# Kernel tuning notes

Measured on AMD Instinct MI355X. Metric: run time of the kernel, lower is better.

Reference implementation:

```python
import jax, jax.numpy as jnp
import numpy as np

B, LS, VS = 4, 1024, 1024
VH, LH, H = 1024, 1024, 16
HD = LH // H  # head_dim = 64


def setup_inputs() -> dict:
    key = jax.random.key(0)
    ks = jax.random.split(key, 10)
    s = 0.02
    return {
        "v_hidden_states": jax.random.normal(ks[0], (B, VS, VH), jnp.float32),
        "l_hidden_states": jax.random.normal(ks[1], (B, LS, LH), jnp.float32),
        "q_w": jax.random.normal(ks[2], (LH, LH), jnp.float32) * s,
        "q_b": jnp.zeros((LH,), jnp.float32),
        "k_w": jax.random.normal(ks[3], (VH, LH), jnp.float32) * s,
        "k_b": jnp.zeros((LH,), jnp.float32),
        "v_w": jax.random.normal(ks[4], (VH, LH), jnp.float32) * s,
        "v_b": jnp.zeros((LH,), jnp.float32),
        "o_w": jax.random.normal(ks[5], (LH, LH), jnp.float32) * s,
        "o_b": jnp.zeros((LH,), jnp.float32),
    }


def reference(v_hidden_states, l_hidden_states, q_w, q_b, k_w, k_b, v_w, v_b, o_w, o_b):
    b, ls, _ = l_hidden_states.shape
    vs = v_hidden_states.shape[1]
    q = (l_hidden_states @ q_w + q_b).reshape(b, ls, H, HD)
    k = (v_hidden_states @ k_w + k_b).reshape(b, vs, H, HD)
    v = (v_hidden_states @ v_w + v_b).reshape(b, vs, H, HD)
    # NOTE: original scales by sqrt(hidden_size), not sqrt(head_dim)
    scale = jnp.sqrt(jnp.asarray(LH, q.dtype))
    scores = jnp.einsum("blhd,bvhd->bhlv", q, k) / scale
    attn = jax.nn.softmax(scores, axis=-1)
    out = jnp.einsum("bhlv,bvhd->blhd", attn, v).reshape(b, ls, LH)
    return out @ o_w + o_b
```

## Files before the change

kernel.cpp:

```cpp
#include <hip/hip_runtime.h>

typedef __bf16 bf16;
typedef __attribute__((ext_vector_type(4))) __bf16 bf16x4;
typedef __attribute__((ext_vector_type(8))) __bf16 bf16x8;
typedef __attribute__((ext_vector_type(4))) float f32x4;

static __device__ __forceinline__ f32x4 mfma_16x16x32(bf16x8 a, bf16x8 b, f32x4 c) {
    return __builtin_amdgcn_mfma_f32_16x16x32_bf16(a, b, c, 0, 0, 0);
}

static __device__ __forceinline__ bf16x8 load8(const float* p) {
    f32x4 a = *(const f32x4*)p;
    f32x4 b = *(const f32x4*)(p + 4);
    bf16x8 r;
    r[0] = (bf16)a[0]; r[1] = (bf16)a[1]; r[2] = (bf16)a[2]; r[3] = (bf16)a[3];
    r[4] = (bf16)b[0]; r[5] = (bf16)b[1]; r[6] = (bf16)b[2]; r[7] = (bf16)b[3];
    return r;
}

static __device__ __forceinline__ void gload_lds16(const void* g, void* l) {
    __builtin_amdgcn_global_load_lds(
        (const __attribute__((address_space(1))) void*)g,
        (__attribute__((address_space(3))) void*)l, 16, 0, 0);
}

#define QSCALE 0.0450842200277801f

#define SYNC_PRE(N)                                                      \
    do {                                                                 \
        asm volatile("s_waitcnt vmcnt(" #N ")" ::: "memory");            \
        __builtin_amdgcn_s_barrier();                                    \
        __builtin_amdgcn_sched_barrier(0);                               \
    } while (0)

#define SYNC_POST()                                                     \
    do {                                                                \
        asm volatile("s_waitcnt lgkmcnt(0)" ::: "memory");              \
        __builtin_amdgcn_sched_barrier(0);                              \
        __builtin_amdgcn_s_barrier();                                   \
    } while (0)

__global__ __launch_bounds__(256) void prep_kernel(
    const float* __restrict__ l_h, const float* __restrict__ v_h,
    const float* __restrict__ w0, const float* __restrict__ w1,
    const float* __restrict__ w2, const float* __restrict__ w3,
    bf16* __restrict__ l_bf, bf16* __restrict__ v_bf,
    bf16* __restrict__ dq, bf16* __restrict__ dkv, bf16* __restrict__ dov)
{
    const int id = blockIdx.x;
    if (id < 4096) {
        const float* s = (id < 2048) ? l_h : v_h;
        bf16*       d = (id < 2048) ? l_bf : v_bf;
        const int   bb = (id < 2048) ? id : id - 2048;
        const size_t i = ((size_t)bb * 256 + threadIdx.x) * 8;
        *(bf16x8*)(d + i) = load8(s + i);
        return;
    }
    const int widx = id - 4096;
    const int z    = widx >> 8;
    const int rem  = widx & 255;
    const int j0   = (rem & 15) * 64;
    const int i0   = (rem >> 4) * 64;
    const float* src; bf16* dst;
    switch (z) {
        case 0:  src = w0; dst = dq; break;
        case 1:  src = w1; dst = dkv; break;
        case 2:  src = w2; dst = dkv + (size_t)1024 * 1024; break;
        default: src = w3; dst = dov; break;
    }
    const float wscale = (z == 0) ? QSCALE : 1.0f;
    __shared__ float T[64][65];
    const int tx = threadIdx.x & 15;
    const int ty = threadIdx.x >> 4;
    #pragma unroll
    for (int it = 0; it < 4; ++it) {
        f32x4 v = *(const f32x4*)(src + (size_t)(i0 + ty + it * 16) * 1024 + j0 + tx * 4);
        T[ty + it * 16][tx * 4 + 0] = v[0];
        T[ty + it * 16][tx * 4 + 1] = v[1];
        T[ty + it * 16][tx * 4 + 2] = v[2];
        T[ty + it * 16][tx * 4 + 3] = v[3];
    }
    __syncthreads();
    #pragma unroll
    for (int it = 0; it < 4; ++it) {
        const int jj = ty + it * 16;
        bf16x4 o;
        o[0] = (bf16)(T[tx * 4 + 0][jj] * wscale);
        o[1] = (bf16)(T[tx * 4 + 1][jj] * wscale);
        o[2] = (bf16)(T[tx * 4 + 2][jj] * wscale);
        o[3] = (bf16)(T[tx * 4 + 3][jj] * wscale);
        *(bf16x4*)(dst + (size_t)(j0 + jj) * 1024 + i0 + tx * 4) = o;
    }
}

__global__ __launch_bounds__(512, 2) void proj256_kernel(
    const bf16* __restrict__ l_bf, const bf16* __restrict__ v_bf,
    const bf16* __restrict__ QWt,  const bf16* __restrict__ KVWt,
    const float* __restrict__ q_b, const float* __restrict__ k_b,
    const float* __restrict__ v_b,
    bf16* __restrict__ Qh, bf16* __restrict__ Kh, bf16* __restrict__ Vt)
{
    __shared__ __align__(16) bf16 Asl[2][256][64];
    __shared__ __align__(16) bf16 Bsl[2][256][64];

    const int t    = threadIdx.x;
    const int lane = t & 63;
    const int wave = t >> 6;
    const int wm   = wave & 1;
    const int wn   = wave >> 1;
    const int l15  = lane & 15;
    const int quad = lane >> 4;
    const int swz  = l15 & 7;

    const int orig = blockIdx.x;
    const int wg   = (orig & 7) * 24 + (orig >> 3);
    const int by   = wg / 12;
    const int bx   = wg - by * 12;

    const bool isQ = bx < 4;
    const bf16* Ap = isQ ? l_bf : v_bf;
    const bf16* Bt = isQ ? QWt  : KVWt;
    const int  gn0 = (isQ ? bx : bx - 4) * 256;
    const int  gm0 = by * 256;

    const int srow8 = t >> 3;
    const int gch   = (t & 7) ^ (srow8 & 7);
    const size_t abase = (size_t)(gm0 + srow8) * 1024 + gch * 8;
    const size_t bbase = (size_t)(gn0 + srow8) * 1024 + gch * 8;

    f32x4 acc[8][4];
    #pragma unroll
    for (int i = 0; i < 8; ++i)
        #pragma unroll
        for (int j = 0; j < 4; ++j)
            acc[i][j] = (f32x4){0.f, 0.f, 0.f, 0.f};

    #define STG(kt_, b_)                                                           \
        {                                                                          \
            _Pragma("unroll")                                                      \
            for (int q = 0; q < 4; ++q)                                            \
                gload_lds16(Ap + abase + (size_t)q * 64 * 1024 + (kt_) * 64,       \
                            &Asl[b_][q * 64 + wave * 8][0]);                       \
            _Pragma("unroll")                                                      \
            for (int q = 0; q < 4; ++q)                                            \
                gload_lds16(Bt + bbase + (size_t)q * 64 * 1024 + (kt_) * 64,       \
                            &Bsl[b_][q * 64 + wave * 8][0]);                       \
        }

    #define CTILE(b_)                                                              \
        {                                                                          \
            bf16x8 bfv[4][2], af[4][2];                                            \
            _Pragma("unroll")                                                      \
            for (int nt = 0; nt < 4; ++nt)                                         \
                _Pragma("unroll")                                                  \
                for (int kk = 0; kk < 2; ++kk)                                     \
                    bfv[nt][kk] = *(const bf16x8*)(&Bsl[b_][wn * 64 + nt * 16 + l15] \
                                                        [((kk * 4 + quad) ^ swz) * 8]); \
            _Pragma("unroll")                                                      \
            for (int i = 0; i < 4; ++i)                                            \
                _Pragma("unroll")                                                  \
                for (int kk = 0; kk < 2; ++kk)                                     \
                    af[i][kk] = *(const bf16x8*)(&Asl[b_][wm * 128 + i * 16 + l15] \
                                                      [((kk * 4 + quad) ^ swz) * 8]); \
            __builtin_amdgcn_s_setprio(1);                                         \
            _Pragma("unroll")                                                      \
            for (int i = 0; i < 4; ++i)                                            \
                _Pragma("unroll")                                                  \
                for (int nt = 0; nt < 4; ++nt)                                     \
                    _Pragma("unroll")                                              \
                    for (int kk = 0; kk < 2; ++kk)                                 \
                        acc[i][nt] = mfma_16x16x32(af[i][kk], bfv[nt][kk], acc[i][nt]); \
            __builtin_amdgcn_s_setprio(0);                                         \
            _Pragma("unroll")                                                      \
            for (int i = 0; i < 4; ++i)                                            \
                _Pragma("unroll")                                                  \
                for (int kk = 0; kk < 2; ++kk)                                     \
                    af[i][kk] = *(const bf16x8*)(&Asl[b_][wm * 128 + 64 + i * 16 + l15] \
                                                      [((kk * 4 + quad) ^ swz) * 8]); \
            __builtin_amdgcn_s_setprio(1);                                         \
            _Pragma("unroll")                                                      \
            for (int i = 0; i < 4; ++i)                                            \
                _Pragma("unroll")                                                  \
                for (int nt = 0; nt < 4; ++nt)                                     \
                    _Pragma("unroll")                                              \
                    for (int kk = 0; kk < 2; ++kk)                                 \
                        acc[4 + i][nt] = mfma_16x16x32(af[i][kk], bfv[nt][kk], acc[4 + i][nt]); \
            __builtin_amdgcn_s_setprio(0);                                         \
        }

    STG(0, 0);
    STG(1, 1);
    asm volatile("s_waitcnt vmcnt(8)" ::: "memory");
    __builtin_amdgcn_s_barrier();

    for (int tt = 0; tt < 14; ++tt) {
        const int b = tt & 1;
        CTILE(b);
        __builtin_amdgcn_s_barrier();
        STG(tt + 2, b);
        asm volatile("s_waitcnt vmcnt(8)" ::: "memory");
        __builtin_amdgcn_s_barrier();
    }
    CTILE(0);
    __builtin_amdgcn_s_barrier();
    asm volatile("s_waitcnt vmcnt(0)" ::: "memory");
    __builtin_amdgcn_s_barrier();
    CTILE(1);

    #undef STG
    #undef CTILE

    #pragma unroll
    for (int nt = 0; nt < 4; ++nt) {
        const int col = gn0 + wn * 64 + nt * 16 + l15;
        float bb; bf16* dst; bool hm;
        if (isQ)             { bb = q_b[col] * QSCALE;   dst = Qh; hm = true;  }
        else if (col < 1024) { bb = k_b[col];            dst = Kh; hm = true;  }
        else                 { bb = v_b[col - 1024];     dst = Vt; hm = false; }
        #pragma unroll
        for (int mt = 0; mt < 8; ++mt) {
            #pragma unroll
            for (int r = 0; r < 4; ++r) {
                const int row = gm0 + wm * 128 + mt * 16 + quad * 4 + r;
                const float v = acc[mt][nt][r] + bb;
                if (hm) {
                    const size_t idx =
                        ((size_t)((row >> 10) * 16 + (col >> 6)) * 1024 +
                         (row & 1023)) * 64 + (col & 63);
                    dst[idx] = (bf16)v;
                } else {
                    const int vc = col - 1024;
                    const size_t idx =
                        ((size_t)((row >> 10) * 16 + (vc >> 6)) * 64 +
                         (vc & 63)) * 1024 + (row & 1023);
                    dst[idx] = (bf16)v;
                }
            }
        }
    }
}

__global__ __launch_bounds__(256, 3) void ogemm_kernel(
    const bf16* __restrict__ Aw, const bf16* __restrict__ OWt,
    const float* __restrict__ o_b, float* __restrict__ C)
{
    __shared__ __align__(16) bf16 As[3][128][32];
    __shared__ __align__(16) bf16 Bs[3][64][32];

    const int t    = threadIdx.x;
    const int lane = t & 63;
    const int wave = t >> 6;
    const int wm   = wave & 1;
    const int wn   = wave >> 1;
    const int l15  = lane & 15;
    const int quad = lane >> 4;

    const int orig = blockIdx.y * 16 + blockIdx.x;
    const int wg   = (orig & 7) * 64 + (orig >> 3);
    const int by   = wg >> 4;
    const int bx   = wg & 15;

    const int gn0 = bx * 64;
    const int gm0 = by * 128;
    const int K   = 1024;

    const int srow    = lane >> 2;
    const int chunk_g = (lane & 3) ^ ((srow >> 1) & 3);
    const size_t aoff = (size_t)(gm0 + wave * 32 + srow) * K + chunk_g * 8;
    const size_t boff = (size_t)(gn0 + wave * 16 + srow) * K + chunk_g * 8;

    f32x4 acc[4][2];
    #pragma unroll
    for (int i = 0; i < 4; ++i)
        #pragma unroll
        for (int j = 0; j < 2; ++j)
            acc[i][j] = (f32x4){0.f, 0.f, 0.f, 0.f};

    #define OSTAGE(k0_, buf_)                                                          \
        {                                                                              \
            gload_lds16(Aw + aoff + (k0_),                  &As[buf_][wave * 32][0]);  \
            gload_lds16(Aw + aoff + (size_t)16 * K + (k0_), &As[buf_][wave * 32 + 16][0]); \
            gload_lds16(OWt + boff + (k0_),                 &Bs[buf_][wave * 16][0]);  \
        }

    #define OCOMPUTE(bufi)                                                             \
        {                                                                              \
            bf16x8 af[4], bfr[2];                                                      \
            _Pragma("unroll")                                                          \
            for (int mt = 0; mt < 4; ++mt) {                                           \
                const int row = wm * 64 + mt * 16 + l15;                               \
                af[mt] = *(const bf16x8*)(&As[bufi][row][(quad ^ ((row >> 1) & 3)) * 8]); \
            }                                                                          \
            _Pragma("unroll")                                                          \
            for (int nt = 0; nt < 2; ++nt) {                                           \
                const int row = wn * 32 + nt * 16 + l15;                               \
                bfr[nt] = *(const bf16x8*)(&Bs[bufi][row][(quad ^ ((row >> 1) & 3)) * 8]); \
            }                                                                          \
            __builtin_amdgcn_s_setprio(1);                                             \
            _Pragma("unroll")                                                          \
            for (int mt = 0; mt < 4; ++mt)                                             \
                _Pragma("unroll")                                                      \
                for (int nt = 0; nt < 2; ++nt)                                         \
                    acc[mt][nt] = mfma_16x16x32(af[mt], bfr[nt], acc[mt][nt]);         \
            __builtin_amdgcn_s_setprio(0);                                             \
        }

    OSTAGE(0, 0);
    OSTAGE(32, 1);
    int bc = 0, bn2 = 2;

    for (int k0 = 0; k0 < K - 64; k0 += 32) {
        OSTAGE(k0 + 64, bn2);
        SYNC_PRE(6);
        OCOMPUTE(bc);
        SYNC_POST();
        int nb = bc + 1;  if (nb == 3) nb = 0;
        int nn = bn2 + 1; if (nn == 3) nn = 0;
        bc = nb; bn2 = nn;
    }
    SYNC_PRE(3);
    OCOMPUTE(bc);
    SYNC_POST();
    bc = (bc + 1 == 3) ? 0 : bc + 1;
    SYNC_PRE(0);
    OCOMPUTE(bc);

    #undef OSTAGE
    #undef OCOMPUTE

    #pragma unroll
    for (int nt = 0; nt < 2; ++nt) {
        const int col = gn0 + wn * 32 + nt * 16 + l15;
        const float bb = o_b[col];
        #pragma unroll
        for (int mt = 0; mt < 4; ++mt) {
            #pragma unroll
            for (int r = 0; r < 4; ++r) {
                const int row = gm0 + wm * 64 + mt * 16 + quad * 4 + r;
                C[(size_t)row * 1024 + col] = acc[mt][nt][r] + bb;
            }
        }
    }
}

__global__ __launch_bounds__(256) void attn_kernel(
    const bf16* __restrict__ Q, const bf16* __restrict__ K,
    const bf16* __restrict__ V, bf16* __restrict__ O)
{
    const int t    = threadIdx.x;
    const int lane = t & 63;
    const int wave = t >> 6;
    const int l15  = lane & 15;
    const int quad = lane >> 4;

    const int head = blockIdx.x;
    const int q0   = blockIdx.y * 128;
    const int b    = head >> 4;
    const int h    = head & 15;

    __shared__ __align__(16) bf16 Kb[2][64][64];
    __shared__ __align__(16) bf16 Vb[2][64][64];
    __shared__ __align__(16) bf16 P[4][32][72];

    const bf16* Qp  = Q + ((size_t)head * 1024 + q0 + wave * 32) * 64;
    const bf16* Kp  = K + (size_t)head * 1024 * 64;
    const bf16* Vtp = V + (size_t)head * 64 * 1024;

    const int r8  = lane >> 3;
    const int c8  = lane & 7;
    const int swz = (c8 ^ r8) * 8;

    bf16x8 aq[2][2];
    #pragma unroll
    for (int mt = 0; mt < 2; ++mt)
        #pragma unroll
        for (int kc = 0; kc < 2; ++kc)
            aq[mt][kc] = *(const bf16x8*)(Qp + (mt * 16 + l15) * 64 + kc * 32 + quad * 8);

    bf16x8 vones;
    #pragma unroll
    for (int j = 0; j < 8; ++j) vones[j] = (bf16)1.0f;

    f32x4 oacc[2][4];
    #pragma unroll
    for (int mt = 0; mt < 2; ++mt)
        #pragma unroll
        for (int nt = 0; nt < 4; ++nt)
            oacc[mt][nt] = (f32x4){0.f, 0.f, 0.f, 0.f};
    f32x4 lacc[2];
    lacc[0] = (f32x4){0.f, 0.f, 0.f, 0.f};
    lacc[1] = (f32x4){0.f, 0.f, 0.f, 0.f};

    #define STAGE(c, buf)                                                          \
        {                                                                          \
            const int kv0_ = (c) * 64;                                             \
            _Pragma("unroll")                                                      \
            for (int g = 0; g < 2; ++g) {                                          \
                const int R = wave * 16 + g * 8;                                   \
                gload_lds16(Kp + (size_t)(kv0_ + R + r8) * 64 + swz,               \
                            &Kb[buf][R][0]);                                       \
                gload_lds16(Vtp + (size_t)(R + r8) * 1024 + kv0_ + swz,            \
                            &Vb[buf][R][0]);                                       \
            }                                                                      \
        }

    STAGE(0, 0);

    const int sw = l15 & 7;

    for (int c = 0; c < 16; ++c) {
        const int buf = c & 1;
        __syncthreads();
        if (c + 1 < 16) STAGE(c + 1, buf ^ 1);

        #pragma unroll
        for (int nt = 0; nt < 4; ++nt) {
            const bf16* krow = &Kb[buf][nt * 16 + l15][0];
            bf16x8 bk0 = *(const bf16x8*)(krow + (quad ^ sw) * 8);
            bf16x8 bk1 = *(const bf16x8*)(krow + ((quad + 4) ^ sw) * 8);
            #pragma unroll
            for (int mt = 0; mt < 2; ++mt) {
                f32x4 s = (f32x4){0.f, 0.f, 0.f, 0.f};
                s = mfma_16x16x32(aq[mt][0], bk0, s);
                s = mfma_16x16x32(aq[mt][1], bk1, s);
                #pragma unroll
                for (int r = 0; r < 4; ++r) {
                    const float e = __builtin_amdgcn_exp2f(s[r]);
                    P[wave][mt * 16 + quad * 4 + r][nt * 16 + l15] = (bf16)e;
                }
            }
        }

        #pragma unroll
        for (int mt = 0; mt < 2; ++mt) {
            bf16x8 pa0 = *(const bf16x8*)(&P[wave][mt * 16 + l15][quad * 8]);
            bf16x8 pa1 = *(const bf16x8*)(&P[wave][mt * 16 + l15][32 + quad * 8]);
            lacc[mt] = mfma_16x16x32(pa0, vones, lacc[mt]);
            lacc[mt] = mfma_16x16x32(pa1, vones, lacc[mt]);
            #pragma unroll
            for (int nt = 0; nt < 4; ++nt) {
                const bf16* vrow = &Vb[buf][nt * 16 + l15][0];
                bf16x8 bv0 = *(const bf16x8*)(vrow + (quad ^ sw) * 8);
                bf16x8 bv1 = *(const bf16x8*)(vrow + ((quad + 4) ^ sw) * 8);
                oacc[mt][nt] = mfma_16x16x32(pa0, bv0, oacc[mt][nt]);
                oacc[mt][nt] = mfma_16x16x32(pa1, bv1, oacc[mt][nt]);
            }
        }
    }
    #undef STAGE

    #pragma unroll
    for (int mt = 0; mt < 2; ++mt) {
        const float invs[4] = {1.0f / lacc[mt][0], 1.0f / lacc[mt][1],
                               1.0f / lacc[mt][2], 1.0f / lacc[mt][3]};
        #pragma unroll
        for (int nt = 0; nt < 4; ++nt) {
            #pragma unroll
            for (int r = 0; r < 4; ++r) {
                const int row = q0 + wave * 32 + mt * 16 + quad * 4 + r;
                O[((size_t)b * 1024 + row) * 1024 + h * 64 + nt * 16 + l15] =
                    (bf16)(oacc[mt][nt][r] * invs[r]);
            }
        }
    }
}

extern "C" void kernel_launch(void* const* d_in, const int* in_sizes, int n_in,
                              void* d_out, int out_size, void* d_ws, size_t ws_size,
                              hipStream_t stream)
{
    const float* v_h = (const float*)d_in[0];
    const float* l_h = (const float*)d_in[1];
    const float* q_w = (const float*)d_in[2];
    const float* q_b = (const float*)d_in[3];
    const float* k_w = (const float*)d_in[4];
    const float* k_b = (const float*)d_in[5];
    const float* v_w = (const float*)d_in[6];
    const float* v_b = (const float*)d_in[7];
    const float* o_w = (const float*)d_in[8];
    const float* o_b = (const float*)d_in[9];
    float* out = (float*)d_out;

    const size_t SZ = (size_t)4096 * 1024;
    const size_t WZ = (size_t)1024 * 1024;

    bf16* l_bf = (bf16*)d_ws;
    bf16* v_bf = l_bf + SZ;
    bf16* QWt  = v_bf + SZ;
    bf16* KVWt = QWt + WZ;
    bf16* OWt  = KVWt + 2 * WZ;
    bf16* Qh   = OWt + WZ;
    bf16* Kh   = Qh + SZ;
    bf16* Vt   = Kh + SZ;
    bf16* Aw   = Vt + SZ;

    prep_kernel<<<dim3(5120), 256, 0, stream>>>(
        l_h, v_h, q_w, k_w, v_w, o_w, l_bf, v_bf, QWt, KVWt, OWt);

    proj256_kernel<<<dim3(192), 512, 0, stream>>>(
        l_bf, v_bf, QWt, KVWt, q_b, k_b, v_b, Qh, Kh, Vt);

    attn_kernel<<<dim3(64, 8), 256, 0, stream>>>(Qh, Kh, Vt, Aw);

    ogemm_kernel<<<dim3(16, 32), 256, 0, stream>>>(Aw, OWt, o_b, out);

    (void)in_sizes; (void)n_in; (void)out_size; (void)ws_size;
}
```

Baseline: 212.0 us.

## Restructure QKV projection GEMM into 8-phase ping-pong schedule with interleaved loads

```diff
diff --git a/kernel.cpp b/kernel.cpp
--- a/kernel.cpp
+++ b/kernel.cpp
@@ -135,80 +135,96 @@
         for (int j = 0; j < 4; ++j)
             acc[i][j] = (f32x4){0.f, 0.f, 0.f, 0.f};
 
-    #define STG(kt_, b_)                                                           \
-        {                                                                          \
-            _Pragma("unroll")                                                      \
-            for (int q = 0; q < 4; ++q)                                            \
-                gload_lds16(Ap + abase + (size_t)q * 64 * 1024 + (kt_) * 64,       \
-                            &Asl[b_][q * 64 + wave * 8][0]);                       \
-            _Pragma("unroll")                                                      \
-            for (int q = 0; q < 4; ++q)                                            \
-                gload_lds16(Bt + bbase + (size_t)q * 64 * 1024 + (kt_) * 64,       \
-                            &Bsl[b_][q * 64 + wave * 8][0]);                       \
-        }
-
-    #define CTILE(b_)                                                              \
-        {                                                                          \
-            bf16x8 bfv[4][2], af[4][2];                                            \
-            _Pragma("unroll")                                                      \
-            for (int nt = 0; nt < 4; ++nt)                                         \
-                _Pragma("unroll")                                                  \
-                for (int kk = 0; kk < 2; ++kk)                                     \
-                    bfv[nt][kk] = *(const bf16x8*)(&Bsl[b_][wn * 64 + nt * 16 + l15] \
-                                                        [((kk * 4 + quad) ^ swz) * 8]); \
-            _Pragma("unroll")                                                      \
-            for (int i = 0; i < 4; ++i)                                            \
-                _Pragma("unroll")                                                  \
-                for (int kk = 0; kk < 2; ++kk)                                     \
-                    af[i][kk] = *(const bf16x8*)(&Asl[b_][wm * 128 + i * 16 + l15] \
-                                                      [((kk * 4 + quad) ^ swz) * 8]); \
-            __builtin_amdgcn_s_setprio(1);                                         \
-            _Pragma("unroll")                                                      \
-            for (int i = 0; i < 4; ++i)                                            \
-                _Pragma("unroll")                                                  \
-                for (int nt = 0; nt < 4; ++nt)                                     \
-                    _Pragma("unroll")                                              \
-                    for (int kk = 0; kk < 2; ++kk)                                 \
-                        acc[i][nt] = mfma_16x16x32(af[i][kk], bfv[nt][kk], acc[i][nt]); \
-            __builtin_amdgcn_s_setprio(0);                                         \
-            _Pragma("unroll")                                                      \
-            for (int i = 0; i < 4; ++i)                                            \
-                _Pragma("unroll")                                                  \
-                for (int kk = 0; kk < 2; ++kk)                                     \
-                    af[i][kk] = *(const bf16x8*)(&Asl[b_][wm * 128 + 64 + i * 16 + l15] \
-                                                      [((kk * 4 + quad) ^ swz) * 8]); \
-            __builtin_amdgcn_s_setprio(1);                                         \
-            _Pragma("unroll")                                                      \
-            for (int i = 0; i < 4; ++i)                                            \
-                _Pragma("unroll")                                                  \
-                for (int nt = 0; nt < 4; ++nt)                                     \
-                    _Pragma("unroll")                                              \
-                    for (int kk = 0; kk < 2; ++kk)                                 \
-                        acc[4 + i][nt] = mfma_16x16x32(af[i][kk], bfv[nt][kk], acc[4 + i][nt]); \
-            __builtin_amdgcn_s_setprio(0);                                         \
-        }
-
-    STG(0, 0);
-    STG(1, 1);
+    #define STGA(kt_, b_)                                                          \
+        { _Pragma("unroll")                                                        \
+          for (int q = 0; q < 4; ++q)                                              \
+              gload_lds16(Ap + abase + (size_t)q * 64 * 1024 + (size_t)(kt_) * 64, \
+                          &Asl[b_][q * 64 + wave * 8][0]); }
+    #define STGB(kt_, b_)                                                          \
+        { _Pragma("unroll")                                                        \
+          for (int q = 0; q < 4; ++q)                                              \
+              gload_lds16(Bt + bbase + (size_t)q * 64 * 1024 + (size_t)(kt_) * 64, \
+                          &Bsl[b_][q * 64 + wave * 8][0]); }
+
+    bf16x8 am[4][2], bn0[2][2], bn1[2][2];
+
+    #define DSA(b_, mh_)                                                           \
+        { _Pragma("unroll")                                                        \
+          for (int i = 0; i < 4; ++i)                                              \
+              _Pragma("unroll")                                                    \
+              for (int kk = 0; kk < 2; ++kk)                                       \
+                  am[i][kk] = *(const bf16x8*)(&Asl[b_][wm * 128 + (mh_) * 64 + i * 16 + l15] \
+                                                    [((kk * 4 + quad) ^ swz) * 8]); }
+    #define DSB(b_, nh_, dst_)                                                     \
+        { _Pragma("unroll")                                                        \
+          for (int j = 0; j < 2; ++j)                                              \
+              _Pragma("unroll")                                                    \
+              for (int kk = 0; kk < 2; ++kk)                                       \
+                  dst_[j][kk] = *(const bf16x8*)(&Bsl[b_][wn * 64 + (nh_) * 32 + j * 16 + l15] \
+                                                      [((kk * 4 + quad) ^ swz) * 8]); }
+
+    #define MM(mh_, nh_, bsrc_)                                                    \
+        { _Pragma("unroll")                                                        \
+          for (int i = 0; i < 4; ++i)                                              \
+              _Pragma("unroll")                                                    \
+              for (int j = 0; j < 2; ++j)                                          \
+                  _Pragma("unroll")                                                 \
+                  for (int kk = 0; kk < 2; ++kk)                                   \
+                      acc[(mh_) * 4 + i][(nh_) * 2 + j] =                          \
+                          mfma_16x16x32(am[i][kk], bsrc_[j][kk],                   \
+                                        acc[(mh_) * 4 + i][(nh_) * 2 + j]); }
+
+    #define BARS_PRE()                                                             \
+        do { __builtin_amdgcn_s_barrier();                                         \
+             asm volatile("s_waitcnt lgkmcnt(0)" ::: "memory");                    \
+             __builtin_amdgcn_sched_barrier(0);                                    \
+             __builtin_amdgcn_s_setprio(1); } while (0)
+    #define BARS_POST()                                                            \
+        do { __builtin_amdgcn_s_setprio(0);                                        \
+             __builtin_amdgcn_sched_barrier(0);                                    \
+             __builtin_amdgcn_s_barrier(); } while (0)
+
+    #define ITER(ta_, STG_EN)                                                      \
+    {                                                                              \
+         DSA(0, 0); DSB(0, 0, bn0);                                        \
+        BARS_PRE(); MM(0, 0, bn0); BARS_POST();                                    \
+         DSB(0, 1, bn1);                                                   \
+        BARS_PRE(); MM(0, 1, bn1); BARS_POST();                                    \
+         DSA(0, 1);                                                        \
+        BARS_PRE(); MM(1, 1, bn1); BARS_POST();                                    \
+         if (STG_EN) { STGA((ta_) + 2, 0);                                 \
+                     asm volatile("s_waitcnt vmcnt(4)" ::: "memory"); }            \
+                 else asm volatile("s_waitcnt vmcnt(0)" ::: "memory");             \
+        BARS_PRE(); MM(1, 0, bn0); BARS_POST();                                    \
+         DSA(1, 0); DSB(1, 0, bn0);                                        \
+        if (STG_EN) STGB((ta_) + 2, 0);                                            \
+        BARS_PRE(); MM(0, 0, bn0); BARS_POST();                                    \
+         DSB(1, 1, bn1);                                                   \
+        BARS_PRE(); MM(0, 1, bn1); BARS_POST();                                    \
+         DSA(1, 1);                                                        \
+        if (STG_EN) STGB((ta_) + 3, 1);                                            \
+        BARS_PRE(); MM(1, 1, bn1); BARS_POST();                                    \
+         if (STG_EN) { STGA((ta_) + 3, 1);                                 \
+                     asm volatile("s_waitcnt vmcnt(8)" ::: "memory"); }            \
+        BARS_PRE(); MM(1, 0, bn0); BARS_POST();                                    \
+    }
+
+    STGA(0, 0); STGB(0, 0); STGB(1, 1); STGA(1, 1);
     asm volatile("s_waitcnt vmcnt(8)" ::: "memory");
     __builtin_amdgcn_s_barrier();
 
-    for (int tt = 0; tt < 14; ++tt) {
-        const int b = tt & 1;
-        CTILE(b);
-        __builtin_amdgcn_s_barrier();
-        STG(tt + 2, b);
-        asm volatile("s_waitcnt vmcnt(8)" ::: "memory");
-        __builtin_amdgcn_s_barrier();
-    }
-    CTILE(0);
-    __builtin_amdgcn_s_barrier();
-    asm volatile("s_waitcnt vmcnt(0)" ::: "memory");
-    __builtin_amdgcn_s_barrier();
-    CTILE(1);
-
-    #undef STG
-    #undef CTILE
+    for (int it = 0; it < 7; ++it)
+        ITER(2 * it, 1)
+    ITER(14, 0)
+
+    #undef ITER
+    #undef BARS_PRE
+    #undef BARS_POST
+    #undef MM
+    #undef DSB
+    #undef DSA
+    #undef STGB
+    #undef STGA
 
     #pragma unroll
     for (int nt = 0; nt < 4; ++nt) {
```

New measurement: 209.6 us. No clear change (-1.2%).
